# Performance work log

Measured on AMD Instinct MI355X. Metric: run time of the kernel, lower is better.

## Reference

```python
import jax, jax.numpy as jnp
import numpy as np

B, S, E = 2, 2048, 2048
H, D = 16, 128  # num_attention_heads, head_dim = hidden_size // num_heads


def rotate_half(x):
    x1 = x[..., : x.shape[-1] // 2]
    x2 = x[..., x.shape[-1] // 2 :]
    return jnp.concatenate((-x2, x1), axis=-1)


def setup_inputs() -> dict:
    key = jax.random.key(0)
    ks = jax.random.split(key, 7)
    return {
        "hidden_states": jax.random.normal(ks[0], (B, S, E), dtype=jnp.float32),
        "cos": jax.random.uniform(ks[1], (1, 1, S, D), dtype=jnp.float32),
        "sin": jax.random.uniform(ks[2], (1, 1, S, D), dtype=jnp.float32),
        "wq": jax.random.normal(ks[3], (E, H * D), dtype=jnp.float32) / np.sqrt(E),
        "wk": jax.random.normal(ks[4], (E, H * D), dtype=jnp.float32) / np.sqrt(E),
        "wv": jax.random.normal(ks[5], (E, H * D), dtype=jnp.float32) / np.sqrt(E),
        "wo": jax.random.normal(ks[6], (H * D, E), dtype=jnp.float32) / np.sqrt(H * D),
    }


def reference(hidden_states, cos, sin, wq, wk, wv, wo):
    # QKV projections (no bias, per attention_bias=False)
    q = (hidden_states @ wq).reshape(B, S, H, D).transpose(0, 2, 1, 3)  # bhsd
    k = (hidden_states @ wk).reshape(B, S, H, D).transpose(0, 2, 1, 3)
    v = (hidden_states @ wv).reshape(B, S, H, D).transpose(0, 2, 1, 3)
    # RoPE (applied after the head transpose, as in the original)
    q = q * cos + rotate_half(q) * sin
    k = k * cos + rotate_half(k) * sin
    # NOTE: original forward never applies self.scaling and uses no causal mask.
    scores = jnp.einsum("bhqd,bhkd->bhqk", q, k)
    attn = jax.nn.softmax(scores.astype(jnp.float32), axis=-1)
    out = jnp.einsum("bhqk,bhkd->bhqd", attn, v)
    out = out.transpose(0, 2, 1, 3).reshape(B, S, H * D)
    return out @ wo
```

## Files before the change

kernel.cpp:

```cpp
#include <hip/hip_runtime.h>
#include <stdint.h>

typedef _Float16 f16;
typedef _Float16 half8 __attribute__((ext_vector_type(8)));
typedef _Float16 half4 __attribute__((ext_vector_type(4)));
typedef __fp16 fp16x2 __attribute__((ext_vector_type(2)));
typedef float f32x4 __attribute__((ext_vector_type(4)));
typedef float f32x16 __attribute__((ext_vector_type(16)));
typedef uint32_t u32x4 __attribute__((ext_vector_type(4)));

static constexpr int Bsz = 2, S = 2048, E = 2048, H = 16, D = 128;
static constexpr int M = Bsz * S;
static constexpr int N_QKV = 3 * H * D;
static constexpr int HD = H * D;

__device__ __forceinline__ void gload_lds16(const void* gp, void* lp) {
  __builtin_amdgcn_global_load_lds(
      (const __attribute__((address_space(1))) uint32_t*)(uintptr_t)gp,
      (__attribute__((address_space(3))) uint32_t*)(uint32_t)(uintptr_t)lp,
      16, 0, 0);
}

__device__ __forceinline__ uint32_t pkrtz(float a, float b) {
  fp16x2 r = __builtin_amdgcn_cvt_pkrtz(a, b);
  return __builtin_bit_cast(uint32_t, r);
}

__global__ void cast_f32_f16(const float* __restrict__ in, f16* __restrict__ out) {
  size_t i = (size_t)(blockIdx.x * 256 + threadIdx.x) * 8;
  float4 a = *(const float4*)&in[i];
  float4 b = *(const float4*)&in[i + 4];
  half8 h;
  h[0] = (f16)a.x; h[1] = (f16)a.y; h[2] = (f16)a.z; h[3] = (f16)a.w;
  h[4] = (f16)b.x; h[5] = (f16)b.y; h[6] = (f16)b.z; h[7] = (f16)b.w;
  *(half8*)&out[i] = h;
}

__global__ void transpose_cast(const float* __restrict__ wq, const float* __restrict__ wk,
                               const float* __restrict__ wv, const float* __restrict__ wo,
                               f16* __restrict__ wt, f16* __restrict__ wot) {
  __shared__ float tile[32][33];
  int z = blockIdx.z;
  const float* src = (z == 0) ? wq : (z == 1) ? wk : (z == 2) ? wv : wo;
  f16* dst = (z == 3) ? wot : wt + (size_t)z * E * HD;
  int bx = blockIdx.x * 32, by = blockIdx.y * 32;
  int tx = threadIdx.x, ty = threadIdx.y;
#pragma unroll
  for (int r = 0; r < 4; ++r)
    tile[ty + r * 8][tx] = src[(size_t)(by + ty + r * 8) * 2048 + bx + tx];
  __syncthreads();
#pragma unroll
  for (int r = 0; r < 4; ++r)
    dst[(size_t)(bx + ty + r * 8) * 2048 + by + tx] = (f16)tile[tx][ty + r * 8];
}

__global__ __launch_bounds__(256, 4) void qkv_fused(const f16* __restrict__ A,
                                                    const f16* __restrict__ Bt,
                                                    const float* __restrict__ cosb,
                                                    const float* __restrict__ sinb,
                                                    f16* __restrict__ Qb,
                                                    f16* __restrict__ Kb,
                                                    f16* __restrict__ VtG) {
  __shared__ f16 lds[16384];
  f16* As = lds;
  f16* Bs = lds + 4096;
  const int Kk = E;
  const int t = threadIdx.x, l = t & 63;
  const int wm = (t >> 7) & 1, wn = (t >> 6) & 1;
  const int bm = blockIdx.x, bn = blockIdx.y;
  const int lr = l & 15, g = l >> 4;
  const int srow = t >> 2;
  const int schunk = t & 3;
  const int scol = ((schunk ^ (srow & 3)) * 8);
  const size_t abase = (size_t)(bm * 128 + srow) * Kk;
  const size_t bbase = (size_t)(bn * 128 + srow) * Kk;
  f32x4 acc[4][4] = {};
  for (int k0 = 0; k0 < Kk; k0 += 32) {
    __syncthreads();
    gload_lds16(&A[abase + k0 + scol], &As[t * 8]);
    gload_lds16(&A[abase + (size_t)64 * Kk + k0 + scol], &As[2048 + t * 8]);
    gload_lds16(&Bt[bbase + k0 + scol], &Bs[t * 8]);
    gload_lds16(&Bt[bbase + (size_t)64 * Kk + k0 + scol], &Bs[2048 + t * 8]);
    __syncthreads();
    half8 af[4], bf[4];
#pragma unroll
    for (int i = 0; i < 4; ++i) {
      int ra = wm * 64 + i * 16 + lr;
      int rb = wn * 64 + i * 16 + lr;
      af[i] = *(const half8*)&As[ra * 32 + ((g ^ (ra & 3)) * 8)];
      bf[i] = *(const half8*)&Bs[rb * 32 + ((g ^ (rb & 3)) * 8)];
    }
#pragma unroll
    for (int i = 0; i < 4; ++i)
#pragma unroll
      for (int j = 0; j < 4; ++j)
        acc[i][j] = __builtin_amdgcn_mfma_f32_16x16x32_f16(af[i], bf[j], acc[i][j], 0, 0, 0);
  }

  const int bt = bn >> 4;
  const int h = bn & 15;
  const int b = bm >> 4;
  const int bh = b * 16 + h;
  const int sblk = (bm & 15) * 128;

  if (bt == 2) {
#pragma unroll
    for (int j = 0; j < 4; ++j) {
      int d = wn * 64 + j * 16 + lr;
      size_t rowb = ((size_t)bh * D + d) * S;
#pragma unroll
      for (int i = 0; i < 4; ++i) {
        int s0 = sblk + wm * 64 + i * 16 + g * 4;
        half4 h4;
#pragma unroll
        for (int r = 0; r < 4; ++r) h4[r] = (f16)acc[i][j][r];
        *(half4*)&VtG[rowb + s0] = h4;
      }
    }
  } else {
    __syncthreads();
#pragma unroll
    for (int i = 0; i < 4; ++i)
#pragma unroll
      for (int j = 0; j < 4; ++j) {
        int row = wm * 64 + i * 16 + g * 4;
        int col = wn * 64 + j * 16 + lr;
#pragma unroll
        for (int r = 0; r < 4; ++r) lds[(row + r) * 128 + col] = (f16)acc[i][j][r];
      }
    __syncthreads();
    f16* Dst = (bt == 0) ? Qb : Kb;
    const int r2 = t >> 1;
    const int sg = sblk + r2;
    const size_t obase = ((size_t)bh * S + sg) * D;
    const size_t cbase = (size_t)sg * D;
#pragma unroll
    for (int k = 0; k < 4; ++k) {
      const int dd0 = (t & 1) * 32 + k * 8;
#pragma unroll
      for (int half = 0; half < 2; ++half) {
        const int dd = dd0 + half * 4;
        float4 cl = *(const float4*)&cosb[cbase + dd];
        float4 ch = *(const float4*)&cosb[cbase + dd + 64];
        float4 sl = *(const float4*)&sinb[cbase + dd];
        float4 sh = *(const float4*)&sinb[cbase + dd + 64];
        half4 lo = *(half4*)&lds[r2 * 128 + dd];
        half4 hv = *(half4*)&lds[r2 * 128 + dd + 64];
        half4 olo, ohi;
        olo[0] = (f16)((float)lo[0] * cl.x - (float)hv[0] * sl.x);
        olo[1] = (f16)((float)lo[1] * cl.y - (float)hv[1] * sl.y);
        olo[2] = (f16)((float)lo[2] * cl.z - (float)hv[2] * sl.z);
        olo[3] = (f16)((float)lo[3] * cl.w - (float)hv[3] * sl.w);
        ohi[0] = (f16)((float)hv[0] * ch.x + (float)lo[0] * sh.x);
        ohi[1] = (f16)((float)hv[1] * ch.y + (float)lo[1] * sh.y);
        ohi[2] = (f16)((float)hv[2] * ch.z + (float)lo[2] * sh.z);
        ohi[3] = (f16)((float)hv[3] * ch.w + (float)lo[3] * sh.w);
        *(half4*)&Dst[obase + dd] = olo;
        *(half4*)&Dst[obase + dd + 64] = ohi;
      }
    }
  }
}

template <typename OutT>
__global__ __launch_bounds__(256, 4) void gemm_bt(const f16* __restrict__ A,
                                                  const f16* __restrict__ Bt,
                                                  OutT* __restrict__ C,
                                                  int Mm, int Nn, int Kk) {
  __shared__ f16 As[128 * 32];
  __shared__ f16 Bs[128 * 32];
  const int t = threadIdx.x, l = t & 63;
  const int wm = (t >> 7) & 1, wn = (t >> 6) & 1;
  const int bm = blockIdx.x, bn = blockIdx.y;
  const int lr = l & 15, g = l >> 4;
  const int srow = t >> 2;
  const int schunk = t & 3;
  const int scol = ((schunk ^ (srow & 3)) * 8);
  const size_t abase = (size_t)(bm * 128 + srow) * Kk;
  const size_t bbase = (size_t)(bn * 128 + srow) * Kk;
  f32x4 acc[4][4] = {};
  for (int k0 = 0; k0 < Kk; k0 += 32) {
    __syncthreads();
    gload_lds16(&A[abase + k0 + scol], &As[t * 8]);
    gload_lds16(&A[abase + (size_t)64 * Kk + k0 + scol], &As[2048 + t * 8]);
    gload_lds16(&Bt[bbase + k0 + scol], &Bs[t * 8]);
    gload_lds16(&Bt[bbase + (size_t)64 * Kk + k0 + scol], &Bs[2048 + t * 8]);
    __syncthreads();
    half8 af[4], bf[4];
#pragma unroll
    for (int i = 0; i < 4; ++i) {
      int ra = wm * 64 + i * 16 + lr;
      int rb = wn * 64 + i * 16 + lr;
      af[i] = *(const half8*)&As[ra * 32 + ((g ^ (ra & 3)) * 8)];
      bf[i] = *(const half8*)&Bs[rb * 32 + ((g ^ (rb & 3)) * 8)];
    }
#pragma unroll
    for (int i = 0; i < 4; ++i)
#pragma unroll
      for (int j = 0; j < 4; ++j)
        acc[i][j] = __builtin_amdgcn_mfma_f32_16x16x32_f16(af[i], bf[j], acc[i][j], 0, 0, 0);
  }
#pragma unroll
  for (int i = 0; i < 4; ++i)
#pragma unroll
    for (int j = 0; j < 4; ++j) {
      int row = bm * 128 + wm * 64 + i * 16 + g * 4;
      int col = bn * 128 + wn * 64 + j * 16 + lr;
#pragma unroll
      for (int r = 0; r < 4; ++r)
        C[(size_t)(row + r) * Nn + col] = (OutT)acc[i][j][r];
    }
}

__device__ __forceinline__ void stage_kv(const f16* __restrict__ Kg, const f16* __restrict__ Vg,
                                         f16* KsB, f16* VsB, int t, int kv) {
#pragma unroll
  for (int rnd = 0; rnd < 4; ++rnd) {
    int row = rnd * 16 + (t >> 4);
    int c = t & 15;
    gload_lds16(&Kg[(size_t)(kv + row) * D + ((c ^ (row & 7)) * 8)], &KsB[rnd * 2048 + t * 8]);
  }
#pragma unroll
  for (int rnd = 0; rnd < 4; ++rnd) {
    int row = rnd * 32 + (t >> 3);
    int c = t & 7;
    gload_lds16(&Vg[(size_t)row * S + kv + ((c ^ (row & 7)) * 8)], &VsB[rnd * 2048 + t * 8]);
  }
}

__global__ __launch_bounds__(256, 2) void flash_attn2(const f16* __restrict__ Q,
                                                      const f16* __restrict__ K,
                                                      const f16* __restrict__ Vt,
                                                      f16* __restrict__ O) {
  __shared__ f16 lds[2][16384];
  const int t = threadIdx.x, l = t & 63, w = t >> 6;
  const int c = l & 31, hi = l >> 5;
  int bid = blockIdx.x;
  bid = (bid & 7) * 64 + (bid >> 3);
  const int bh = bid >> 4, qt = bid & 15;
  const size_t baseQ = (size_t)bh * S * D;
  const f16* Kg = K + baseQ;
  const f16* Vg = Vt + (size_t)bh * D * S;
  const int q0 = qt * 128 + w * 32;
  half8 qf[8];
#pragma unroll
  for (int dc = 0; dc < 8; ++dc)
    qf[dc] = *(const half8*)&Q[baseQ + (size_t)(q0 + c) * D + dc * 16 + hi * 8];
  f32x16 o[4] = {};
  float m = -3.0e38f, ssum = 0.f;

  stage_kv(Kg, Vg, &lds[0][0], &lds[0][8192], t, 0);
  __syncthreads();

  for (int it = 0; it < S / 64; ++it) {
    const int cur = it & 1;
    const f16* KsB = &lds[cur][0];
    const f16* VsB = &lds[cur][8192];
    if (it + 1 < S / 64) stage_kv(Kg, Vg, &lds[cur ^ 1][0], &lds[cur ^ 1][8192], t, (it + 1) * 64);

    f32x16 s0 = {}, s1 = {};
    __builtin_amdgcn_s_setprio(1);
#pragma unroll
    for (int dc = 0; dc < 8; ++dc) {
      const int r0 = c, r1 = 32 + c;
      half8 kf0 = *(const half8*)&KsB[r0 * 128 + (((2 * dc + hi) ^ (r0 & 7)) * 8)];
      half8 kf1 = *(const half8*)&KsB[r1 * 128 + (((2 * dc + hi) ^ (r1 & 7)) * 8)];
      s0 = __builtin_amdgcn_mfma_f32_32x32x16_f16(kf0, qf[dc], s0, 0, 0, 0);
      s1 = __builtin_amdgcn_mfma_f32_32x32x16_f16(kf1, qf[dc], s1, 0, 0, 0);
    }
    __builtin_amdgcn_s_setprio(0);

    float tm = s0[0];
#pragma unroll
    for (int r = 1; r < 16; ++r) tm = fmaxf(tm, s0[r]);
#pragma unroll
    for (int r = 0; r < 16; ++r) tm = fmaxf(tm, s1[r]);
    tm = fmaxf(tm, __shfl_xor(tm, 32));
    float mn = fmaxf(m, tm);
    float corr = __expf(m - mn);
    m = mn;
    float ts = 0.f;
#pragma unroll
    for (int r = 0; r < 16; ++r) { s0[r] = __expf(s0[r] - mn); ts += s0[r]; }
#pragma unroll
    for (int r = 0; r < 16; ++r) { s1[r] = __expf(s1[r] - mn); ts += s1[r]; }
    ts += __shfl_xor(ts, 32);
    ssum = ssum * corr + ts;
#pragma unroll
    for (int dt = 0; dt < 4; ++dt)
#pragma unroll
      for (int r = 0; r < 16; ++r) o[dt][r] *= corr;

    half8 pf[4];
#pragma unroll
    for (int ks = 0; ks < 4; ++ks) {
      const int B0 = 2 * (ks & 1), B1 = B0 + 1;
      uint32_t X0, X1, Y0, Y1;
      if (ks < 2) {
        X0 = pkrtz(s0[4 * B0 + 0], s0[4 * B0 + 1]);
        X1 = pkrtz(s0[4 * B0 + 2], s0[4 * B0 + 3]);
        Y0 = pkrtz(s0[4 * B1 + 0], s0[4 * B1 + 1]);
        Y1 = pkrtz(s0[4 * B1 + 2], s0[4 * B1 + 3]);
      } else {
        X0 = pkrtz(s1[4 * B0 + 0], s1[4 * B0 + 1]);
        X1 = pkrtz(s1[4 * B0 + 2], s1[4 * B0 + 3]);
        Y0 = pkrtz(s1[4 * B1 + 0], s1[4 * B1 + 1]);
        Y1 = pkrtz(s1[4 * B1 + 2], s1[4 * B1 + 3]);
      }
      asm volatile("v_permlane32_swap_b32 %0, %1" : "+v"(X0), "+v"(Y0));
      asm volatile("v_permlane32_swap_b32 %0, %1" : "+v"(X1), "+v"(Y1));
      u32x4 pw; pw[0] = X0; pw[1] = X1; pw[2] = Y0; pw[3] = Y1;
      pf[ks] = __builtin_bit_cast(half8, pw);
    }

    __builtin_amdgcn_s_setprio(1);
#pragma unroll
    for (int dt = 0; dt < 4; ++dt) {
      const int row = dt * 32 + c;
#pragma unroll
      for (int ks = 0; ks < 4; ++ks) {
        half8 vf = *(const half8*)&VsB[row * 64 + (((2 * ks + hi) ^ (row & 7)) * 8)];
        o[dt] = __builtin_amdgcn_mfma_f32_32x32x16_f16(vf, pf[ks], o[dt], 0, 0, 0);
      }
    }
    __builtin_amdgcn_s_setprio(0);
    __syncthreads();
  }

  const float inv = 1.f / ssum;
  const int b = bh >> 4, h = bh & 15;
  const size_t orow = ((size_t)(b * S + q0 + c)) * HD + h * D;
#pragma unroll
  for (int dt = 0; dt < 4; ++dt)
#pragma unroll
    for (int b2 = 0; b2 < 4; ++b2) {
      half4 h4;
#pragma unroll
      for (int a = 0; a < 4; ++a) h4[a] = (f16)(o[dt][4 * b2 + a] * inv);
      *(half4*)&O[orow + dt * 32 + 8 * b2 + 4 * hi] = h4;
    }
}

extern "C" void kernel_launch(void* const* d_in, const int* in_sizes, int n_in,
                              void* d_out, int out_size, void* d_ws, size_t ws_size,
                              hipStream_t stream) {
  (void)in_sizes; (void)n_in; (void)out_size; (void)ws_size;
  const float* hs = (const float*)d_in[0];
  const float* cosb = (const float*)d_in[1];
  const float* sinb = (const float*)d_in[2];
  const float* wq = (const float*)d_in[3];
  const float* wk = (const float*)d_in[4];
  const float* wv = (const float*)d_in[5];
  const float* wo = (const float*)d_in[6];
  float* out = (float*)d_out;
  char* ws = (char*)d_ws;
  f16* hs16 = (f16*)(ws);
  f16* attn = (f16*)(ws);
  f16* wt   = (f16*)(ws + (16u << 20));
  f16* wot  = (f16*)(ws + (40u << 20));
  f16* Qb   = (f16*)(ws + (48u << 20));
  f16* Kb   = (f16*)(ws + (64u << 20));
  f16* VtG  = (f16*)(ws + (80u << 20));

  cast_f32_f16<<<dim3(4096), dim3(256), 0, stream>>>(hs, hs16);
  transpose_cast<<<dim3(64, 64, 4), dim3(32, 8), 0, stream>>>(wq, wk, wv, wo, wt, wot);
  qkv_fused<<<dim3(32, 48), dim3(256), 0, stream>>>(hs16, wt, cosb, sinb, Qb, Kb, VtG);
  flash_attn2<<<dim3(512), dim3(256), 0, stream>>>(Qb, Kb, VtG, attn);
  gemm_bt<float><<<dim3(32, 16), dim3(256), 0, stream>>>(attn, wot, out, M, E, HD);
}
```

Before: 312.2 us.

## Apply RoPE directly from registers in QKV GEMM and remap block order

The Q/K path of the fused QKV GEMM now remaps which B columns each wave owns, so every thread holds matching d and d+64 accumulator pairs. RoPE is then applied straight from registers, which removes the 32 KB LDS staging buffer and its two barriers. LDS per block shrinks to 16 KB, which can raise occupancy. The grid is flattened to 1D with an XCD-aware swizzle of block ids, which changes L2 locality. The cost is duplicated main-loop code, and the store pattern may be less coalesced, since each lane writes scattered rows.

```diff
diff --git a/kernel.cpp b/kernel.cpp
--- a/kernel.cpp
+++ b/kernel.cpp
@@ -61,49 +61,99 @@
                                                     f16* __restrict__ Qb,
                                                     f16* __restrict__ Kb,
                                                     f16* __restrict__ VtG) {
-  __shared__ f16 lds[16384];
-  f16* As = lds;
-  f16* Bs = lds + 4096;
+  __shared__ f16 As[4096];
+  __shared__ f16 Bs[4096];
   const int Kk = E;
   const int t = threadIdx.x, l = t & 63;
   const int wm = (t >> 7) & 1, wn = (t >> 6) & 1;
-  const int bm = blockIdx.x, bn = blockIdx.y;
   const int lr = l & 15, g = l >> 4;
+  int bid = blockIdx.x;
+  int wg = (bid & 7) * 192 + (bid >> 3);
+  const int bn = wg / 32, bm = wg % 32;
   const int srow = t >> 2;
-  const int schunk = t & 3;
-  const int scol = ((schunk ^ (srow & 3)) * 8);
+  const int scol = (((t & 3) ^ (srow & 3)) * 8);
   const size_t abase = (size_t)(bm * 128 + srow) * Kk;
   const size_t bbase = (size_t)(bn * 128 + srow) * Kk;
-  f32x4 acc[4][4] = {};
-  for (int k0 = 0; k0 < Kk; k0 += 32) {
-    __syncthreads();
-    gload_lds16(&A[abase + k0 + scol], &As[t * 8]);
-    gload_lds16(&A[abase + (size_t)64 * Kk + k0 + scol], &As[2048 + t * 8]);
-    gload_lds16(&Bt[bbase + k0 + scol], &Bs[t * 8]);
-    gload_lds16(&Bt[bbase + (size_t)64 * Kk + k0 + scol], &Bs[2048 + t * 8]);
-    __syncthreads();
-    half8 af[4], bf[4];
-#pragma unroll
-    for (int i = 0; i < 4; ++i) {
-      int ra = wm * 64 + i * 16 + lr;
-      int rb = wn * 64 + i * 16 + lr;
-      af[i] = *(const half8*)&As[ra * 32 + ((g ^ (ra & 3)) * 8)];
-      bf[i] = *(const half8*)&Bs[rb * 32 + ((g ^ (rb & 3)) * 8)];
-    }
-#pragma unroll
-    for (int i = 0; i < 4; ++i)
-#pragma unroll
-      for (int j = 0; j < 4; ++j)
-        acc[i][j] = __builtin_amdgcn_mfma_f32_16x16x32_f16(af[i], bf[j], acc[i][j], 0, 0, 0);
-  }
-
   const int bt = bn >> 4;
   const int h = bn & 15;
   const int b = bm >> 4;
   const int bh = b * 16 + h;
   const int sblk = (bm & 15) * 128;
-
-  if (bt == 2) {
+  f32x4 acc[4][4] = {};
+
+  if (bt < 2) {
+    for (int k0 = 0; k0 < Kk; k0 += 32) {
+      __syncthreads();
+      gload_lds16(&A[abase + k0 + scol], &As[t * 8]);
+      gload_lds16(&A[abase + (size_t)64 * Kk + k0 + scol], &As[2048 + t * 8]);
+      gload_lds16(&Bt[bbase + k0 + scol], &Bs[t * 8]);
+      gload_lds16(&Bt[bbase + (size_t)64 * Kk + k0 + scol], &Bs[2048 + t * 8]);
+      __syncthreads();
+      half8 af[4], bf[4];
+#pragma unroll
+      for (int i = 0; i < 4; ++i) {
+        int ra = wm * 64 + i * 16 + lr;
+        af[i] = *(const half8*)&As[ra * 32 + ((g ^ (ra & 3)) * 8)];
+      }
+#pragma unroll
+      for (int j = 0; j < 4; ++j) {
+        int rb = wn * 32 + (j & 1) * 16 + (j >> 1) * 64 + lr;
+        bf[j] = *(const half8*)&Bs[rb * 32 + ((g ^ (rb & 3)) * 8)];
+      }
+#pragma unroll
+      for (int i = 0; i < 4; ++i)
+#pragma unroll
+        for (int j = 0; j < 4; ++j)
+          acc[i][j] = __builtin_amdgcn_mfma_f32_16x16x32_f16(bf[j], af[i], acc[i][j], 0, 0, 0);
+    }
+    f16* Dst = (bt == 0) ? Qb : Kb;
+#pragma unroll
+    for (int i = 0; i < 4; ++i) {
+      const int s = sblk + wm * 64 + i * 16 + lr;
+      const size_t obase = ((size_t)bh * S + s) * D;
+      const size_t cbase = (size_t)s * D;
+#pragma unroll
+      for (int j = 0; j < 2; ++j) {
+        const int dlo = wn * 32 + j * 16 + g * 4;
+        float4 cl = *(const float4*)&cosb[cbase + dlo];
+        float4 ch = *(const float4*)&cosb[cbase + dlo + 64];
+        float4 sl = *(const float4*)&sinb[cbase + dlo];
+        float4 sh = *(const float4*)&sinb[cbase + dlo + 64];
+        float cla[4] = {cl.x, cl.y, cl.z, cl.w}, cha[4] = {ch.x, ch.y, ch.z, ch.w};
+        float sla[4] = {sl.x, sl.y, sl.z, sl.w}, sha[4] = {sh.x, sh.y, sh.z, sh.w};
+        half4 olo, ohi;
+#pragma unroll
+        for (int r = 0; r < 4; ++r) {
+          float xl = acc[i][j][r], xh = acc[i][j + 2][r];
+          olo[r] = (f16)(xl * cla[r] - xh * sla[r]);
+          ohi[r] = (f16)(xh * cha[r] + xl * sha[r]);
+        }
+        *(half4*)&Dst[obase + dlo] = olo;
+        *(half4*)&Dst[obase + dlo + 64] = ohi;
+      }
+    }
+  } else {
+    for (int k0 = 0; k0 < Kk; k0 += 32) {
+      __syncthreads();
+      gload_lds16(&A[abase + k0 + scol], &As[t * 8]);
+      gload_lds16(&A[abase + (size_t)64 * Kk + k0 + scol], &As[2048 + t * 8]);
+      gload_lds16(&Bt[bbase + k0 + scol], &Bs[t * 8]);
+      gload_lds16(&Bt[bbase + (size_t)64 * Kk + k0 + scol], &Bs[2048 + t * 8]);
+      __syncthreads();
+      half8 af[4], bf[4];
+#pragma unroll
+      for (int i = 0; i < 4; ++i) {
+        int ra = wm * 64 + i * 16 + lr;
+        int rb = wn * 64 + i * 16 + lr;
+        af[i] = *(const half8*)&As[ra * 32 + ((g ^ (ra & 3)) * 8)];
+        bf[i] = *(const half8*)&Bs[rb * 32 + ((g ^ (rb & 3)) * 8)];
+      }
+#pragma unroll
+      for (int i = 0; i < 4; ++i)
+#pragma unroll
+        for (int j = 0; j < 4; ++j)
+          acc[i][j] = __builtin_amdgcn_mfma_f32_16x16x32_f16(af[i], bf[j], acc[i][j], 0, 0, 0);
+    }
 #pragma unroll
     for (int j = 0; j < 4; ++j) {
       int d = wn * 64 + j * 16 + lr;
@@ -115,48 +165,6 @@
 #pragma unroll
         for (int r = 0; r < 4; ++r) h4[r] = (f16)acc[i][j][r];
         *(half4*)&VtG[rowb + s0] = h4;
-      }
-    }
-  } else {
-    __syncthreads();
-#pragma unroll
-    for (int i = 0; i < 4; ++i)
-#pragma unroll
-      for (int j = 0; j < 4; ++j) {
-        int row = wm * 64 + i * 16 + g * 4;
-        int col = wn * 64 + j * 16 + lr;
-#pragma unroll
-        for (int r = 0; r < 4; ++r) lds[(row + r) * 128 + col] = (f16)acc[i][j][r];
-      }
-    __syncthreads();
-    f16* Dst = (bt == 0) ? Qb : Kb;
-    const int r2 = t >> 1;
-    const int sg = sblk + r2;
-    const size_t obase = ((size_t)bh * S + sg) * D;
-    const size_t cbase = (size_t)sg * D;
-#pragma unroll
-    for (int k = 0; k < 4; ++k) {
-      const int dd0 = (t & 1) * 32 + k * 8;
-#pragma unroll
-      for (int half = 0; half < 2; ++half) {
-        const int dd = dd0 + half * 4;
-        float4 cl = *(const float4*)&cosb[cbase + dd];
-        float4 ch = *(const float4*)&cosb[cbase + dd + 64];
-        float4 sl = *(const float4*)&sinb[cbase + dd];
-        float4 sh = *(const float4*)&sinb[cbase + dd + 64];
-        half4 lo = *(half4*)&lds[r2 * 128 + dd];
-        half4 hv = *(half4*)&lds[r2 * 128 + dd + 64];
-        half4 olo, ohi;
-        olo[0] = (f16)((float)lo[0] * cl.x - (float)hv[0] * sl.x);
-        olo[1] = (f16)((float)lo[1] * cl.y - (float)hv[1] * sl.y);
-        olo[2] = (f16)((float)lo[2] * cl.z - (float)hv[2] * sl.z);
-        olo[3] = (f16)((float)lo[3] * cl.w - (float)hv[3] * sl.w);
-        ohi[0] = (f16)((float)hv[0] * ch.x + (float)lo[0] * sh.x);
-        ohi[1] = (f16)((float)hv[1] * ch.y + (float)lo[1] * sh.y);
-        ohi[2] = (f16)((float)hv[2] * ch.z + (float)lo[2] * sh.z);
-        ohi[3] = (f16)((float)hv[3] * ch.w + (float)lo[3] * sh.w);
-        *(half4*)&Dst[obase + dd] = olo;
-        *(half4*)&Dst[obase + dd + 64] = ohi;
       }
     }
   }
@@ -364,7 +372,7 @@
 
   cast_f32_f16<<<dim3(4096), dim3(256), 0, stream>>>(hs, hs16);
   transpose_cast<<<dim3(64, 64, 4), dim3(32, 8), 0, stream>>>(wq, wk, wv, wo, wt, wot);
-  qkv_fused<<<dim3(32, 48), dim3(256), 0, stream>>>(hs16, wt, cosb, sinb, Qb, Kb, VtG);
+  qkv_fused<<<dim3(1536), dim3(256), 0, stream>>>(hs16, wt, cosb, sinb, Qb, Kb, VtG);
   flash_attn2<<<dim3(512), dim3(256), 0, stream>>>(Qb, Kb, VtG, attn);
   gemm_bt<float><<<dim3(32, 16), dim3(256), 0, stream>>>(attn, wot, out, M, E, HD);
 }
```

Measured after the change: 304.3 us. -2.5%, faster.
